# Performance work log

Hardware: AMD Instinct MI355X
Metric: run time of the kernel (lower is better)

The kernel has to match this reference:

```python
import jax, jax.numpy as jnp
from jax import lax
import numpy as np

# Mamba2 config from PixelMamba.__init__
D_MODEL = 128; D_STATE = 256; D_CONV = 4; EXPAND = 4; HEADDIM = 32
D_INNER = EXPAND * D_MODEL              # 512
NHEADS = D_INNER // HEADDIM             # 16
NGROUPS = 1
D_XBC = D_INNER + 2 * NGROUPS * D_STATE # 1024 (conv channels)
D_IN_PROJ = 2 * D_INNER + 2 * NGROUPS * D_STATE + NHEADS  # 1552
CHUNK = 128                             # SSD chunk length


def setup_inputs() -> dict:
    key = jax.random.key(0)
    ks = jax.random.split(key, 10)
    Bb, C, H, W = 2, 3, 64, 64
    f32 = jnp.float32
    rn = lambda k, shape, s: jax.random.normal(k, shape, f32) * s
    return {
        "x": jax.random.normal(ks[0], (Bb, C, H, W), f32),
        "fc0_w": rn(ks[1], (3, D_MODEL), 1.0 / np.sqrt(3.0)),
        "fc0_b": rn(ks[2], (D_MODEL,), 0.01),
        "in_proj_w": rn(ks[3], (D_MODEL, D_IN_PROJ), 1.0 / np.sqrt(D_MODEL)),
        "conv_w": rn(ks[4], (D_XBC, D_CONV), 1.0 / np.sqrt(D_CONV)),
        "conv_b": rn(ks[5], (D_XBC,), 0.01),
        "dt_bias": jnp.log(jnp.expm1(jax.random.uniform(ks[6], (NHEADS,), f32, 0.001, 0.1))),
        "A_log": jnp.log(jax.random.uniform(ks[7], (NHEADS,), f32, 1.0, 16.0)),
        "D": rn(ks[8], (NHEADS,), 1.0),
        "norm_w": jnp.ones((D_INNER,), f32),
        "out_proj_w": rn(ks[9], (D_INNER, D_MODEL), 1.0 / np.sqrt(D_INNER)),
    }


def _mamba2(u, in_proj_w, conv_w, conv_b, dt_bias, A_log, D, norm_w, out_proj_w):
    # u: (B, L, d_model)
    Bb, L, _ = u.shape
    zxbcdt = u @ in_proj_w                                     # (B,L,1552)
    z = zxbcdt[..., :D_INNER]                                  # gate
    xBC = zxbcdt[..., D_INNER:D_INNER + D_XBC]
    dt = jax.nn.softplus(zxbcdt[..., -NHEADS:] + dt_bias)     # (B,L,H)

    # causal depthwise conv1d + SiLU
    xc = lax.conv_general_dilated(
        xBC.transpose(0, 2, 1), conv_w[:, None, :], (1,), [(D_CONV - 1, 0)],
        dimension_numbers=('NCH', 'OIH', 'NCH'), feature_group_count=D_XBC)
    xBC = jax.nn.silu(xc + conv_b[None, :, None]).transpose(0, 2, 1)

    xs = xBC[..., :D_INNER].reshape(Bb, L, NHEADS, HEADDIM)    # (B,L,H,P)
    Bm = xBC[..., D_INNER:D_INNER + D_STATE]                   # (B,L,N), ngroups=1
    Cm = xBC[..., D_INNER + D_STATE:]                          # (B,L,N)
    A = -jnp.exp(A_log)                                        # (H,) negative

    # ---- SSD chunked selective scan ----
    NC = L // CHUNK
    a = (dt * A).reshape(Bb, NC, CHUNK, NHEADS)                # log-decay per step (<=0)
    dt_r = dt.reshape(Bb, NC, CHUNK, NHEADS)
    x_r = xs.reshape(Bb, NC, CHUNK, NHEADS, HEADDIM)
    B_r = Bm.reshape(Bb, NC, CHUNK, D_STATE)
    C_r = Cm.reshape(Bb, NC, CHUNK, D_STATE)
    cum = jnp.cumsum(a, axis=2)                                # (B,NC,Q,H)

    # intra-chunk quadratic part: attn[t,s] = (C_t.B_s) * exp(cum_t - cum_s) * dt_s, s<=t
    mask = jnp.tril(jnp.ones((CHUNK, CHUNK), bool))
    diff = cum[:, :, :, None, :] - cum[:, :, None, :, :]       # (B,NC,t,s,H)
    decay = jnp.exp(jnp.where(mask[None, None, :, :, None], diff, -jnp.inf))
    CB = jnp.einsum('bctn,bcsn->bcts', C_r, B_r)
    attn = CB[..., None] * decay * dt_r[:, :, None, :, :]      # (B,NC,t,s,H)
    y_intra = jnp.einsum('bctsh,bcshp->bcthp', attn, x_r)

    # per-chunk end states: sum_s exp(cum_end - cum_s) dt_s x_s B_s^T
    decay_end = jnp.exp(cum[:, :, -1:, :] - cum)               # (B,NC,Q,H)
    states = jnp.einsum('bcsh,bcsn,bcshp->bchpn', decay_end * dt_r, B_r, x_r)

    # inter-chunk recurrence over NC chunks (small sequential scan)
    chunk_decay = jnp.exp(cum[:, :, -1, :])                    # (B,NC,H)
    def step(S, inp):
        cd, st = inp
        return S * cd[..., None, None] + st, S                 # emit state BEFORE chunk
    S0 = jnp.zeros((Bb, NHEADS, HEADDIM, D_STATE), u.dtype)
    _, prev = lax.scan(step, S0, (chunk_decay.transpose(1, 0, 2),
                                  states.transpose(1, 0, 2, 3, 4)))
    prev = prev.transpose(1, 0, 2, 3, 4)                       # (B,NC,H,P,N)
    y_inter = jnp.einsum('bcth,bctn,bchpn->bcthp', jnp.exp(cum), C_r, prev)

    y = (y_intra + y_inter).reshape(Bb, L, NHEADS, HEADDIM) + D[None, None, :, None] * xs
    y = y.reshape(Bb, L, D_INNER)

    # gated RMSNorm (norm_before_gate=False): norm(y * silu(z)) * w
    y = y * jax.nn.silu(z)
    y = y * lax.rsqrt(jnp.mean(y * y, axis=-1, keepdims=True) + 1e-5) * norm_w
    return y @ out_proj_w


def reference(x, fc0_w, fc0_b, in_proj_w, conv_w, conv_b, dt_bias, A_log, D, norm_w, out_proj_w):
    Bb, C, H, W = x.shape
    x1 = x.transpose(0, 2, 3, 1).reshape(Bb, -1, C)            # raster order
    x2 = x[:, :, ::-1, ::-1].transpose(0, 2, 3, 1).reshape(Bb, -1, C)  # flipped
    u = jnp.concatenate([x1, x2], axis=1) @ fc0_w + fc0_b      # (B, 2HW, 128)
    return _mamba2(u, in_proj_w, conv_w, conv_b, dt_bias, A_log, D, norm_w, out_proj_w)
```

## Files before the change

### kernel.cpp

```cpp
#include <hip/hip_runtime.h>

typedef short short8 __attribute__((ext_vector_type(8)));
typedef float f32x4 __attribute__((ext_vector_type(4)));
typedef unsigned short ushort;
typedef unsigned int uint;

#define MFMA16(a,b,c) __builtin_amdgcn_mfma_f32_16x16x32_bf16(a,b,c,0,0,0)
#define DPROJ 1552

constexpr size_t OFF_M    = 0;
constexpr size_t OFF_CB_B = 0x5000;
constexpr size_t OFF_WT   = 0x8000;
constexpr size_t OFF_XT   = 0x30000;
constexpr size_t OFF_DT   = OFF_XT  + 16777216ull;
constexpr size_t OFF_BCM  = OFF_DT  + 1048576ull;
constexpr size_t OFF_CUM  = OFF_BCM + 16777216ull;
constexpr size_t OFF_CDC  = OFF_CUM + 1048576ull;
constexpr size_t OFF_CBT  = OFF_CDC + 8192ull;
constexpr size_t OFF_BT   = OFF_CBT + 4194304ull;
constexpr size_t OFF_ST   = OFF_BT  + 8388608ull;
constexpr size_t OFF_Y    = OFF_ST  + 33554432ull;

__device__ __forceinline__ float sigm(float x){ return 1.0f/(1.0f + __expf(-x)); }
__device__ __forceinline__ ushort f2bf(float f){
  union { float f; uint u; } c; c.f = f;
  uint u = c.u;
  return (ushort)((u + 0x7FFFu + ((u>>16)&1u)) >> 16);
}
__device__ __forceinline__ float bf2f(ushort h){
  union { uint u; float f; } c; c.u = ((uint)h)<<16;
  return c.f;
}
__device__ __forceinline__ void swz2048(int p, int& bc, int& h){
  int xcd = p & 7, slot = p >> 3;
  bc = xcd*16 + (slot >> 4);
  h  = slot & 15;
}

__global__ __launch_bounds__(256) void k0_prep(const float* __restrict__ fc0_w,
                                               const float* __restrict__ fc0_b,
                                               const float* __restrict__ W,
                                               char* __restrict__ wsb){
  float* Mo = (float*)(wsb + OFF_M);
  float* Co = (float*)(wsb + OFF_CB_B);
  int j = blockIdx.x*256 + threadIdx.x;
  if (j >= DPROJ) return;
  float m0=0.f,m1=0.f,m2=0.f,cc=0.f;
  for (int d=0; d<128; ++d){
    float w = W[(size_t)d*DPROJ + j];
    m0 = fmaf(fc0_w[d],     w, m0);
    m1 = fmaf(fc0_w[128+d], w, m1);
    m2 = fmaf(fc0_w[256+d], w, m2);
    cc = fmaf(fc0_b[d],     w, cc);
  }
  Mo[j] = m0; Mo[DPROJ + j] = m1; Mo[2*DPROJ + j] = m2;
  Co[j] = cc;
}

__global__ __launch_bounds__(256) void k0b_wt(const float* __restrict__ norm_w,
                                              const float* __restrict__ Wout,
                                              char* __restrict__ wsb){
  ushort* WT = (ushort*)(wsb + OFF_WT);
  int d = blockIdx.x;
  for (int i = threadIdx.x; i < 512; i += 256)
    WT[(size_t)d*512 + i] = f2bf(norm_w[i]*Wout[(size_t)i*128 + d]);
}

__device__ __forceinline__ void proj8(int li, const float* __restrict__ xb,
                                      const float* m0, const float* m1, const float* m2,
                                      const float* c8, float* dst){
  if (li < 0){
    #pragma unroll
    for (int j=0;j<8;++j) dst[j] = 0.f;
    return;
  }
  int hh, wv;
  if (li < 4096){ hh = li>>6; wv = li&63; }
  else { int l2 = li-4096; hh = 63-(l2>>6); wv = 63-(l2&63); }
  float x0 = xb[hh*64+wv], x1 = xb[4096+hh*64+wv], x2 = xb[8192+hh*64+wv];
  #pragma unroll
  for (int j=0;j<8;++j)
    dst[j] = fmaf(x2, m2[j], fmaf(x1, m1[j], fmaf(x0, m0[j], c8[j])));
}

__device__ __forceinline__ void conv8(const float* cb8, const float* cw0, const float* cw1,
                                      const float* cw2, const float* cw3,
                                      const float* wA, const float* wB,
                                      const float* wC, const float* wD, ushort* o){
  #pragma unroll
  for (int j=0;j<8;++j){
    float a = cb8[j];
    a = fmaf(wA[j], cw0[j], a);
    a = fmaf(wB[j], cw1[j], a);
    a = fmaf(wC[j], cw2[j], a);
    a = fmaf(wD[j], cw3[j], a);
    o[j] = f2bf(a * sigm(a));
  }
}
__device__ __forceinline__ void cp8(ushort* d, const ushort* s){
  #pragma unroll
  for (int j=0;j<8;++j) d[j] = s[j];
}

__global__ __launch_bounds__(256) void k12_projconv(const float* __restrict__ x,
                                                    const float* __restrict__ conv_w,
                                                    const float* __restrict__ conv_b,
                                                    char* __restrict__ wsb){
  int tid = threadIdx.x;
  int cg = tid & 127, rl = tid >> 7;
  int row0 = blockIdx.x*16 + rl*8;
  int b = row0 >> 13, l0 = row0 & 8191;
  const float* M  = (const float*)(wsb + OFF_M);
  const float* Cc = (const float*)(wsb + OFF_CB_B);
  const float* xb = x + (size_t)b*12288;
  int ch0 = cg*8, j0 = 512 + ch0;
  float m0[8],m1[8],m2[8],c8[8],cw0[8],cw1[8],cw2[8],cw3[8],cb8[8];
  #pragma unroll
  for (int j=0;j<8;++j){
    m0[j]=M[j0+j]; m1[j]=M[DPROJ+j0+j]; m2[j]=M[2*DPROJ+j0+j]; c8[j]=Cc[j0+j];
    cw0[j]=conv_w[(ch0+j)*4+0]; cw1[j]=conv_w[(ch0+j)*4+1];
    cw2[j]=conv_w[(ch0+j)*4+2]; cw3[j]=conv_w[(ch0+j)*4+3];
    cb8[j]=conv_b[ch0+j];
  }
  bool is_xs = (ch0 < 512);
  ushort* bcmp = (ushort*)(wsb + OFF_BCM);
  int chb = ch0 - 512;
  uint colw[8][4];
  ushort oprev[8];
  float w0[8],w1[8],w2[8],w3[8];
  ushort o[8];
  proj8(l0-3, xb, m0,m1,m2,c8, w1);
  proj8(l0-2, xb, m0,m1,m2,c8, w2);
  proj8(l0-1, xb, m0,m1,m2,c8, w3);

#define ROW_EVEN(R, WN, WA, WB, WC)                                          \
  proj8(l0+R, xb, m0,m1,m2,c8, WN);                                          \
  conv8(cb8,cw0,cw1,cw2,cw3, WA,WB,WC,WN, o);                                \
  if (is_xs) cp8(oprev, o);                                                  \
  else *(uint4*)(bcmp + (size_t)(row0+R)*512 + chb) = *(uint4*)o;
#define ROW_ODD(R, WN, WA, WB, WC)                                           \
  proj8(l0+R, xb, m0,m1,m2,c8, WN);                                          \
  conv8(cb8,cw0,cw1,cw2,cw3, WA,WB,WC,WN, o);                                \
  if (is_xs){ _Pragma("unroll")                                              \
    for (int j=0;j<8;++j) colw[j][(R)>>1] = (uint)oprev[j] | ((uint)o[j]<<16); } \
  else *(uint4*)(bcmp + (size_t)(row0+R)*512 + chb) = *(uint4*)o;

  ROW_EVEN(0, w0, w1,w2,w3)
  ROW_ODD (1, w1, w2,w3,w0)
  ROW_EVEN(2, w2, w3,w0,w1)
  ROW_ODD (3, w3, w0,w1,w2)
  ROW_EVEN(4, w0, w1,w2,w3)
  ROW_ODD (5, w1, w2,w3,w0)
  ROW_EVEN(6, w2, w3,w0,w1)
  ROW_ODD (7, w3, w0,w1,w2)
#undef ROW_EVEN
#undef ROW_ODD

  if (is_xs){
    int h = ch0>>5, p0 = ch0&31;
    int bc = row0>>7, grp = (row0&127)>>3;
    ushort* dst = (ushort*)(wsb+OFF_XT) + (((size_t)(bc*16+h)*16 + grp)*32)*8;
    #pragma unroll
    for (int j=0;j<8;++j){
      uint4 v; v.x = colw[j][0]; v.y = colw[j][1]; v.z = colw[j][2]; v.w = colw[j][3];
      *(uint4*)(dst + (size_t)(p0+j)*8) = v;
    }
  }
}

__global__ __launch_bounds__(128) void k3_cum(const float* __restrict__ x,
                                              const float* __restrict__ dt_bias,
                                              const float* __restrict__ A_log,
                                              char* __restrict__ wsb){
  int bi = blockIdx.x;
  int h = bi & 15; int bc = bi >> 4;
  int t = threadIdx.x;
  int r = bc*128 + t;
  int b = r >> 13, l = r & 8191;
  int hp, wv;
  if (l < 4096){ hp = l>>6; wv = l&63; }
  else { int l2 = l-4096; hp = 63-(l2>>6); wv = 63-(l2&63); }
  const float* xb = x + (size_t)b*12288;
  float x0 = xb[hp*64+wv], x1 = xb[4096+hp*64+wv], x2 = xb[8192+hp*64+wv];
  const float* M  = (const float*)(wsb + OFF_M);
  const float* Cc = (const float*)(wsb + OFF_CB_B);
  int j = 1536 + h;
  float v = Cc[j];
  v = fmaf(x0, M[j], v);
  v = fmaf(x1, M[DPROJ+j], v);
  v = fmaf(x2, M[2*DPROJ+j], v);
  float tt = v + dt_bias[h];
  float dtv = (tt > 20.f) ? tt : log1pf(__expf(tt));
  ((float*)(wsb+OFF_DT))[(size_t)r*16 + h] = dtv;
  __shared__ float s[128];
  float A = -__expf(A_log[h]);
  s[t] = dtv * A; __syncthreads();
  for (int off=1; off<128; off<<=1){
    float sv = (t>=off) ? s[t-off] : 0.f;
    __syncthreads();
    s[t] += sv;
    __syncthreads();
  }
  ((float*)(wsb + OFF_CUM))[(size_t)bi*128 + t] = s[t];
  if (t==127) ((float*)(wsb + OFF_CDC))[bi] = __expf(s[127]);
}

__global__ __launch_bounds__(256) void k4a_cb(char* __restrict__ wsb){
  int bi = blockIdx.x;
  int sq = bi & 3; int bc = bi >> 2;
  __shared__ __align__(16) char sC[16384];
  __shared__ __align__(16) char sB[4096];
  const ushort* bcm = (const ushort*)(wsb + OFF_BCM);
  ushort* cbtT = (ushort*)(wsb + OFF_CBT) + (size_t)bc*16384;
  ushort* btb  = (ushort*)(wsb + OFF_BT)  + (size_t)bc*32768;
  size_t rb = (size_t)bc*128;
  int tid = threadIdx.x;
  int lane = tid&63, wid = tid>>6, l15 = lane&15, l4 = lane>>4;
  int s_base = sq*32;
  f32x4 acc[2][2] = {};
  for (int nt = 0; nt < 4; ++nt){
    int n0 = nt*64;
    __syncthreads();
    for (int idx = tid; idx < 1024; idx += 256){
      int t = idx>>3, c = idx&7;
      uint4 v = *(const uint4*)(bcm + (rb+t)*512 + 256 + n0 + c*8);
      *(uint4*)(sC + ((t*128 + c*16) ^ ((t&7)<<4))) = v;
    }
    {
      int idx = tid;
      int s = idx>>3, c = idx&7;
      uint4 v = *(const uint4*)(bcm + (rb+s_base+s)*512 + n0 + c*8);
      *(uint4*)(sB + ((s*128 + c*16) ^ ((s&7)<<4))) = v;
    }
    __syncthreads();
    {
      int grp_l = tid>>6, n_l = tid&63;
      ushort o[8];
      #pragma unroll
      for (int sj=0; sj<8; ++sj){
        int sl = grp_l*8 + sj;
        o[sj] = *(const ushort*)(sB + ((sl*128 + n_l*2) ^ ((sl&7)<<4)));
      }
      *(uint4*)(btb + (size_t)((sq*4+grp_l)*256 + n0 + n_l)*8) = *(uint4*)o;
    }
    #pragma unroll
    for (int ks = 0; ks < 2; ++ks){
      int kb = ks*64 + l4*16;
      int t0 = wid*32 + l15, t1 = t0 + 16;
      short8 a0 = *(const short8*)(sC + ((t0*128 + kb) ^ ((t0&7)<<4)));
      short8 a1 = *(const short8*)(sC + ((t1*128 + kb) ^ ((t1&7)<<4)));
      short8 b0 = *(const short8*)(sB + ((l15*128 + kb) ^ ((l15&7)<<4)));
      short8 b1 = *(const short8*)(sB + (((16+l15)*128 + kb) ^ (((16+l15)&7)<<4)));
      acc[0][0] = MFMA16(a0,b0,acc[0][0]);
      acc[0][1] = MFMA16(a0,b1,acc[0][1]);
      acc[1][0] = MFMA16(a1,b0,acc[1][0]);
      acc[1][1] = MFMA16(a1,b1,acc[1][1]);
    }
  }
  #pragma unroll
  for (int mt=0; mt<2; ++mt)
  #pragma unroll
  for (int st=0; st<2; ++st)
  #pragma unroll
  for (int r=0; r<4; ++r){
    int t = wid*32 + mt*16 + l4*4 + r;
    int s = s_base + st*16 + l15;
    cbtT[(size_t)((s>>3)*128 + t)*8 + (s&7)] = f2bf(acc[mt][st][r]);
  }
}

__global__ __launch_bounds__(256) void k4s_states(char* __restrict__ wsb){
  int bc, h; swz2048(blockIdx.x, bc, h);
  int bi = bc*16 + h;
  __shared__ float sW[128];
  const ushort* xt  = (const ushort*)(wsb + OFF_XT) + (size_t)bi*4096;
  const ushort* btb = (const ushort*)(wsb + OFF_BT) + (size_t)bc*32768;
  const float* cum  = (const float*)(wsb + OFF_CUM) + (size_t)bi*128;
  const float* dtp  = (const float*)(wsb + OFF_DT);
  ushort* st = (ushort*)(wsb + OFF_ST) + (size_t)bi*8192;
  size_t rb = (size_t)bc*128;
  int tid = threadIdx.x;
  if (tid < 128){
    float c127 = cum[127];
    sW[tid] = __expf(c127 - cum[tid]) * dtp[(rb+tid)*16 + h];
  }
  __syncthreads();
  int lane = tid&63, wid = tid>>6, l15 = lane&15, l4 = lane>>4;
  f32x4 acc2[2][4] = {};
  #pragma unroll
  for (int ks = 0; ks < 4; ++ks){
    int grp = ks*4 + l4;
    const float* wp = sW + grp*8;
    short8 ra0 = *(const short8*)(xt + (size_t)(grp*32 + l15)*8);
    short8 ra1 = *(const short8*)(xt + (size_t)(grp*32 + 16 + l15)*8);
    short8 a0, a1;
    #pragma unroll
    for (int j=0;j<8;++j){
      a0[j] = (short)f2bf(bf2f((ushort)ra0[j]) * wp[j]);
      a1[j] = (short)f2bf(bf2f((ushort)ra1[j]) * wp[j]);
    }
    #pragma unroll
    for (int ntl = 0; ntl < 4; ++ntl){
      int n = wid*64 + ntl*16 + l15;
      short8 b = *(const short8*)(btb + (size_t)(grp*256 + n)*8);
      acc2[0][ntl] = MFMA16(a0,b,acc2[0][ntl]);
      acc2[1][ntl] = MFMA16(a1,b,acc2[1][ntl]);
    }
  }
  #pragma unroll
  for (int mt=0; mt<2; ++mt)
  #pragma unroll
  for (int ntl=0; ntl<4; ++ntl)
  #pragma unroll
  for (int r=0; r<4; ++r){
    int p = mt*16 + l4*4 + r;
    int n = wid*64 + ntl*16 + l15;
    st[(size_t)((n>>3)*32 + p)*8 + (n&7)] = f2bf(acc2[mt][ntl][r]);
  }
}

__global__ __launch_bounds__(256) void k5_scan(char* __restrict__ wsb){
  int g = blockIdx.x*256 + threadIdx.x;
  int l = g & 63;
  int e = l & 7, plow = l >> 3;
  int up = g >> 6;
  int p = (up & 3)*8 + plow; up >>= 2;
  int grp = up & 31; up >>= 5;
  int h = up & 15; int b = up >> 4;
  int off = (grp*32 + p)*8 + e;
  ushort* st = (ushort*)(wsb + OFF_ST);
  const float* cdc = (const float*)(wsb + OFF_CDC);
  float S = 0.f;
  for (int c=0; c<64; ++c){
    int bi = (b*64+c)*16 + h;
    size_t idx = (size_t)bi*8192 + off;
    float v = bf2f(st[idx]);
    st[idx] = f2bf(S);
    S = fmaf(S, cdc[bi], v);
  }
}

__global__ __launch_bounds__(256) void k4y_out(const float* __restrict__ Dp,
                                               char* __restrict__ wsb){
  int bc, h; swz2048(blockIdx.x, bc, h);
  int bi = bc*16 + h;
  __shared__ float sCum[128], sDt[128], sE[128];
  const ushort* cbt = (const ushort*)(wsb + OFF_CBT) + (size_t)bc*16384;
  const ushort* xt  = (const ushort*)(wsb + OFF_XT) + (size_t)bi*4096;
  const ushort* bcm = (const ushort*)(wsb + OFF_BCM);
  const ushort* prev= (const ushort*)(wsb + OFF_ST) + (size_t)bi*8192;
  const float* cum  = (const float*)(wsb + OFF_CUM) + (size_t)bi*128;
  const float* dtp  = (const float*)(wsb + OFF_DT);
  ushort* Yb = (ushort*)(wsb + OFF_Y);
  size_t rb = (size_t)bc*128;
  int tid = threadIdx.x;
  if (tid < 128){
    float cv = cum[tid];
    sCum[tid] = cv;
    sDt[tid]  = dtp[(rb+tid)*16 + h];
    sE[tid]   = __expf(cv);
  }
  __syncthreads();
  int lane = tid&63, wid = tid>>6, l15 = lane&15, l4 = lane>>4;
  int t0 = wid*32 + l15, t1 = t0 + 16;
  float ct0 = sCum[t0], ct1 = sCum[t1];
  f32x4 acc[2][2] = {};
  #pragma unroll
  for (int ks = 0; ks < 4; ++ks){
    int grp = ks*4 + l4;
    int s0 = grp*8;
    short8 ra0 = *(const short8*)(cbt + (size_t)(grp*128 + t0)*8);
    short8 ra1 = *(const short8*)(cbt + (size_t)(grp*128 + t1)*8);
    short8 a0, a1;
    #pragma unroll
    for (int j=0;j<8;++j){
      int s = s0 + j;
      float cs = sCum[s], ds = sDt[s];
      float e0 = __expf(fminf(ct0 - cs, 0.f)) * ds;
      float e1 = __expf(fminf(ct1 - cs, 0.f)) * ds;
      float v0 = (t0 >= s) ? bf2f((ushort)ra0[j]) * e0 : 0.f;
      float v1 = (t1 >= s) ? bf2f((ushort)ra1[j]) * e1 : 0.f;
      a0[j] = (short)f2bf(v0);
      a1[j] = (short)f2bf(v1);
    }
    short8 b0 = *(const short8*)(xt + (size_t)(grp*32 + l15)*8);
    short8 b1 = *(const short8*)(xt + (size_t)(grp*32 + 16 + l15)*8);
    acc[0][0] = MFMA16(a0,b0,acc[0][0]);
    acc[0][1] = MFMA16(a0,b1,acc[0][1]);
    acc[1][0] = MFMA16(a1,b0,acc[1][0]);
    acc[1][1] = MFMA16(a1,b1,acc[1][1]);
  }
  f32x4 acc2[2][2] = {};
  #pragma unroll
  for (int ks = 0; ks < 8; ++ks){
    int koff = ks*32 + l4*8;
    int grp = ks*4 + l4;
    short8 a0 = *(const short8*)(bcm + (rb+t0)*512 + 256 + koff);
    short8 a1 = *(const short8*)(bcm + (rb+t1)*512 + 256 + koff);
    short8 b0 = *(const short8*)(prev + (size_t)(grp*32 + l15)*8);
    short8 b1 = *(const short8*)(prev + (size_t)(grp*32 + 16 + l15)*8);
    acc2[0][0] = MFMA16(a0,b0,acc2[0][0]);
    acc2[0][1] = MFMA16(a0,b1,acc2[0][1]);
    acc2[1][0] = MFMA16(a1,b0,acc2[1][0]);
    acc2[1][1] = MFMA16(a1,b1,acc2[1][1]);
  }
  float Dh = Dp[h];
  #pragma unroll
  for (int mt=0; mt<2; ++mt){
    int tb = wid*32 + mt*16 + l4*4;
    int tg = tb>>3, e0 = tb&7;
    #pragma unroll
    for (int nt=0; nt<2; ++nt){
      int p = nt*16 + l15;
      ushort xv[4];
      *(uint2*)xv = *(const uint2*)(xt + (size_t)(tg*32 + p)*8 + e0);
      #pragma unroll
      for (int r=0; r<4; ++r){
        int t = tb + r;
        float yv = acc[mt][nt][r] + sE[t]*acc2[mt][nt][r] + Dh*bf2f(xv[r]);
        Yb[(rb+t)*512 + h*32 + p] = f2bf(yv);
      }
    }
  }
}

__global__ __launch_bounds__(256) void k7_final(const float* __restrict__ x,
                                                char* __restrict__ wsb,
                                                float* __restrict__ out){
  int r0 = blockIdx.x*32;
  __shared__ __align__(16) char sG[32768];
  __shared__ float sScale[32];
  const ushort* Yb = (const ushort*)(wsb + OFF_Y);
  const float* M  = (const float*)(wsb + OFF_M);
  const float* Cb = (const float*)(wsb + OFF_CB_B);
  const ushort* WT = (const ushort*)(wsb + OFF_WT);
  int tid = threadIdx.x;
  int r = tid>>3, li = tid&7;
  int row = r0 + r; int b = row>>13, l = row & 8191;
  int hh, wv;
  if (l < 4096){ hh = l>>6; wv = l&63; }
  else { int l2 = l-4096; hh = 63-(l2>>6); wv = 63-(l2&63); }
  const float* xb = x + (size_t)b*12288;
  float x0 = xb[hh*64+wv], x1 = xb[4096+hh*64+wv], x2 = xb[8192+hh*64+wv];
  float sq = 0.f;
  #pragma unroll
  for (int k = 0; k < 8; ++k){
    int i0 = li*64 + k*8;
    short8 yv = *(const short8*)(Yb + (size_t)row*512 + i0);
    ushort g8[8];
    #pragma unroll
    for (int j=0;j<8;++j){
      int i = i0 + j;
      float z = Cb[i];
      z = fmaf(x0, M[i], z);
      z = fmaf(x1, M[DPROJ+i], z);
      z = fmaf(x2, M[2*DPROJ+i], z);
      float g = bf2f((ushort)yv[j]) * z * sigm(z);
      sq = fmaf(g, g, sq);
      g8[j] = f2bf(g);
    }
    *(uint4*)(sG + ((r*1024 + i0*2) ^ ((r&7)<<4))) = *(uint4*)g8;
  }
  sq += __shfl_xor(sq, 1, 64);
  sq += __shfl_xor(sq, 2, 64);
  sq += __shfl_xor(sq, 4, 64);
  if (li == 0) sScale[r] = rsqrtf(sq*(1.f/512.f) + 1e-5f);
  __syncthreads();
  int lane = tid&63, wid = tid>>6, l15 = lane&15, l4 = lane>>4;
  f32x4 acc[2][2] = {};
  #pragma unroll
  for (int ks = 0; ks < 16; ++ks){
    int kb = ks*64 + l4*16;
    int rr0 = l15, rr1 = 16+l15;
    short8 a0 = *(const short8*)(sG + ((rr0*1024 + kb) ^ ((rr0&7)<<4)));
    short8 a1 = *(const short8*)(sG + ((rr1*1024 + kb) ^ ((rr1&7)<<4)));
    int koff = ks*32 + l4*8;
    short8 b0 = *(const short8*)(WT + (size_t)(wid*32 + l15)*512 + koff);
    short8 b1 = *(const short8*)(WT + (size_t)(wid*32 + 16 + l15)*512 + koff);
    acc[0][0] = MFMA16(a0,b0,acc[0][0]);
    acc[0][1] = MFMA16(a0,b1,acc[0][1]);
    acc[1][0] = MFMA16(a1,b0,acc[1][0]);
    acc[1][1] = MFMA16(a1,b1,acc[1][1]);
  }
  #pragma unroll
  for (int mt=0; mt<2; ++mt)
  #pragma unroll
  for (int nt=0; nt<2; ++nt)
  #pragma unroll
  for (int r4=0; r4<4; ++r4){
    int rr = mt*16 + l4*4 + r4;
    int d = wid*32 + nt*16 + l15;
    out[(size_t)(r0+rr)*128 + d] = acc[mt][nt][r4] * sScale[rr];
  }
}

extern "C" void kernel_launch(void* const* d_in, const int* in_sizes, int n_in,
                              void* d_out, int out_size, void* d_ws, size_t ws_size,
                              hipStream_t stream) {
  const float* x         = (const float*)d_in[0];
  const float* fc0_w     = (const float*)d_in[1];
  const float* fc0_b     = (const float*)d_in[2];
  const float* in_proj_w = (const float*)d_in[3];
  const float* conv_w    = (const float*)d_in[4];
  const float* conv_b    = (const float*)d_in[5];
  const float* dt_bias   = (const float*)d_in[6];
  const float* A_log     = (const float*)d_in[7];
  const float* Dp        = (const float*)d_in[8];
  const float* norm_w    = (const float*)d_in[9];
  const float* out_proj_w= (const float*)d_in[10];
  char* wsb  = (char*)d_ws;
  float* out = (float*)d_out;

  k0_prep<<<dim3(7),     dim3(256), 0, stream>>>(fc0_w, fc0_b, in_proj_w, wsb);
  k0b_wt <<<dim3(128),   dim3(256), 0, stream>>>(norm_w, out_proj_w, wsb);
  k12_projconv<<<dim3(1024), dim3(256), 0, stream>>>(x, conv_w, conv_b, wsb);
  k3_cum <<<dim3(2048),  dim3(128), 0, stream>>>(x, dt_bias, A_log, wsb);
  k4a_cb <<<dim3(512),   dim3(256), 0, stream>>>(wsb);
  k4s_states<<<dim3(2048), dim3(256), 0, stream>>>(wsb);
  k5_scan<<<dim3(1024),  dim3(256), 0, stream>>>(wsb);
  k4y_out<<<dim3(2048),  dim3(256), 0, stream>>>(Dp, wsb);
  k7_final<<<dim3(512),  dim3(256), 0, stream>>>(x, wsb, out);
}
```

Baseline: 152.8 us.

## Fuse chunk-state, inter-chunk scan and inter-chunk output into one sequential kernel

Replaces the separate chunk-state kernel, the global-memory scan kernel and the inter-chunk output matmul with one kernel, kscan. Each block (batch, head, half of headdim) walks all 64 chunks in order. It keeps the running state in fp32 shared memory and writes y_inter directly, so the 32MB bf16 state round trip and the separate prev-state pass go away. The B-transpose layout is now written in k12_projconv instead of k4a_cb. The cost is that the sequential loop runs on only 64 blocks, which leaves most CUs idle and exposes per-chunk load latency and barrier latency 64 times in a row.

```diff
diff --git a/kernel.cpp b/kernel.cpp
--- a/kernel.cpp
+++ b/kernel.cpp
@@ -97,10 +97,6 @@
     o[j] = f2bf(a * sigm(a));
   }
 }
-__device__ __forceinline__ void cp8(ushort* d, const ushort* s){
-  #pragma unroll
-  for (int j=0;j<8;++j) d[j] = s[j];
-}
 
 __global__ __launch_bounds__(256) void k12_projconv(const float* __restrict__ x,
                                                     const float* __restrict__ conv_w,
@@ -123,6 +119,8 @@
     cb8[j]=conv_b[ch0+j];
   }
   bool is_xs = (ch0 < 512);
+  bool is_b  = (ch0 >= 512) && (ch0 < 768);
+  bool pack  = is_xs || is_b;
   ushort* bcmp = (ushort*)(wsb + OFF_BCM);
   int chb = ch0 - 512;
   uint colw[8][4];
@@ -136,14 +134,15 @@
 #define ROW_EVEN(R, WN, WA, WB, WC)                                          \
   proj8(l0+R, xb, m0,m1,m2,c8, WN);                                          \
   conv8(cb8,cw0,cw1,cw2,cw3, WA,WB,WC,WN, o);                                \
-  if (is_xs) cp8(oprev, o);                                                  \
-  else *(uint4*)(bcmp + (size_t)(row0+R)*512 + chb) = *(uint4*)o;
+  if (pack){ _Pragma("unroll")                                               \
+    for (int j=0;j<8;++j) oprev[j] = o[j]; }                                 \
+  if (!is_xs) *(uint4*)(bcmp + (size_t)(row0+R)*512 + chb) = *(uint4*)o;
 #define ROW_ODD(R, WN, WA, WB, WC)                                           \
   proj8(l0+R, xb, m0,m1,m2,c8, WN);                                          \
   conv8(cb8,cw0,cw1,cw2,cw3, WA,WB,WC,WN, o);                                \
-  if (is_xs){ _Pragma("unroll")                                              \
+  if (pack){ _Pragma("unroll")                                               \
     for (int j=0;j<8;++j) colw[j][(R)>>1] = (uint)oprev[j] | ((uint)o[j]<<16); } \
-  else *(uint4*)(bcmp + (size_t)(row0+R)*512 + chb) = *(uint4*)o;
+  if (!is_xs) *(uint4*)(bcmp + (size_t)(row0+R)*512 + chb) = *(uint4*)o;
 
   ROW_EVEN(0, w0, w1,w2,w3)
   ROW_ODD (1, w1, w2,w3,w0)
@@ -156,14 +155,21 @@
 #undef ROW_EVEN
 #undef ROW_ODD
 
+  int bc = row0>>7, grp = (row0&127)>>3;
   if (is_xs){
     int h = ch0>>5, p0 = ch0&31;
-    int bc = row0>>7, grp = (row0&127)>>3;
     ushort* dst = (ushort*)(wsb+OFF_XT) + (((size_t)(bc*16+h)*16 + grp)*32)*8;
     #pragma unroll
     for (int j=0;j<8;++j){
       uint4 v; v.x = colw[j][0]; v.y = colw[j][1]; v.z = colw[j][2]; v.w = colw[j][3];
       *(uint4*)(dst + (size_t)(p0+j)*8) = v;
+    }
+  } else if (is_b){
+    ushort* btb = (ushort*)(wsb+OFF_BT) + (size_t)bc*32768;
+    #pragma unroll
+    for (int j=0;j<8;++j){
+      uint4 v; v.x = colw[j][0]; v.y = colw[j][1]; v.z = colw[j][2]; v.w = colw[j][3];
+      *(uint4*)(btb + (size_t)(grp*256 + chb + j)*8) = v;
     }
   }
 }
@@ -212,7 +218,6 @@
   __shared__ __align__(16) char sB[4096];
   const ushort* bcm = (const ushort*)(wsb + OFF_BCM);
   ushort* cbtT = (ushort*)(wsb + OFF_CBT) + (size_t)bc*16384;
-  ushort* btb  = (ushort*)(wsb + OFF_BT)  + (size_t)bc*32768;
   size_t rb = (size_t)bc*128;
   int tid = threadIdx.x;
   int lane = tid&63, wid = tid>>6, l15 = lane&15, l4 = lane>>4;
@@ -233,16 +238,6 @@
       *(uint4*)(sB + ((s*128 + c*16) ^ ((s&7)<<4))) = v;
     }
     __syncthreads();
-    {
-      int grp_l = tid>>6, n_l = tid&63;
-      ushort o[8];
-      #pragma unroll
-      for (int sj=0; sj<8; ++sj){
-        int sl = grp_l*8 + sj;
-        o[sj] = *(const ushort*)(sB + ((sl*128 + n_l*2) ^ ((sl&7)<<4)));
-      }
-      *(uint4*)(btb + (size_t)((sq*4+grp_l)*256 + n0 + n_l)*8) = *(uint4*)o;
-    }
     #pragma unroll
     for (int ks = 0; ks < 2; ++ks){
       int kb = ks*64 + l4*16;
@@ -269,74 +264,85 @@
   }
 }
 
-__global__ __launch_bounds__(256) void k4s_states(char* __restrict__ wsb){
-  int bc, h; swz2048(blockIdx.x, bc, h);
-  int bi = bc*16 + h;
-  __shared__ float sW[128];
-  const ushort* xt  = (const ushort*)(wsb + OFF_XT) + (size_t)bi*4096;
-  const ushort* btb = (const ushort*)(wsb + OFF_BT) + (size_t)bc*32768;
-  const float* cum  = (const float*)(wsb + OFF_CUM) + (size_t)bi*128;
+__global__ __launch_bounds__(512) void kscan(char* __restrict__ wsb){
+  int blk = blockIdx.x;
+  int ph = blk & 1, h = (blk>>1)&15, b = blk>>5;
+  __shared__ float sS[4096];
+  __shared__ __align__(16) char sSb[8192];
+  __shared__ float sW[128], sE[128];
+  const ushort* xtb = (const ushort*)(wsb + OFF_XT);
+  const ushort* btb0= (const ushort*)(wsb + OFF_BT);
+  const ushort* bcm = (const ushort*)(wsb + OFF_BCM);
+  const float* cumb = (const float*)(wsb + OFF_CUM);
   const float* dtp  = (const float*)(wsb + OFF_DT);
-  ushort* st = (ushort*)(wsb + OFF_ST) + (size_t)bi*8192;
-  size_t rb = (size_t)bc*128;
+  const float* cdcp = (const float*)(wsb + OFF_CDC);
+  ushort* YI = (ushort*)(wsb + OFF_ST);
   int tid = threadIdx.x;
-  if (tid < 128){
-    float c127 = cum[127];
-    sW[tid] = __expf(c127 - cum[tid]) * dtp[(rb+tid)*16 + h];
-  }
+  int lane = tid&63, wave = tid>>6, l15 = lane&15, l4 = lane>>4;
+  for (int i = tid; i < 4096; i += 512) sS[i] = 0.f;
+  for (int i = tid; i < 4096; i += 512) ((ushort*)sSb)[i] = 0;
   __syncthreads();
-  int lane = tid&63, wid = tid>>6, l15 = lane&15, l4 = lane>>4;
-  f32x4 acc2[2][4] = {};
-  #pragma unroll
-  for (int ks = 0; ks < 4; ++ks){
-    int grp = ks*4 + l4;
-    const float* wp = sW + grp*8;
-    short8 ra0 = *(const short8*)(xt + (size_t)(grp*32 + l15)*8);
-    short8 ra1 = *(const short8*)(xt + (size_t)(grp*32 + 16 + l15)*8);
-    short8 a0, a1;
-    #pragma unroll
-    for (int j=0;j<8;++j){
-      a0[j] = (short)f2bf(bf2f((ushort)ra0[j]) * wp[j]);
-      a1[j] = (short)f2bf(bf2f((ushort)ra1[j]) * wp[j]);
-    }
-    #pragma unroll
-    for (int ntl = 0; ntl < 4; ++ntl){
-      int n = wid*64 + ntl*16 + l15;
-      short8 b = *(const short8*)(btb + (size_t)(grp*256 + n)*8);
-      acc2[0][ntl] = MFMA16(a0,b,acc2[0][ntl]);
-      acc2[1][ntl] = MFMA16(a1,b,acc2[1][ntl]);
-    }
-  }
-  #pragma unroll
-  for (int mt=0; mt<2; ++mt)
-  #pragma unroll
-  for (int ntl=0; ntl<4; ++ntl)
-  #pragma unroll
-  for (int r=0; r<4; ++r){
-    int p = mt*16 + l4*4 + r;
-    int n = wid*64 + ntl*16 + l15;
-    st[(size_t)((n>>3)*32 + p)*8 + (n&7)] = f2bf(acc2[mt][ntl][r]);
-  }
-}
-
-__global__ __launch_bounds__(256) void k5_scan(char* __restrict__ wsb){
-  int g = blockIdx.x*256 + threadIdx.x;
-  int l = g & 63;
-  int e = l & 7, plow = l >> 3;
-  int up = g >> 6;
-  int p = (up & 3)*8 + plow; up >>= 2;
-  int grp = up & 31; up >>= 5;
-  int h = up & 15; int b = up >> 4;
-  int off = (grp*32 + p)*8 + e;
-  ushort* st = (ushort*)(wsb + OFF_ST);
-  const float* cdc = (const float*)(wsb + OFF_CDC);
-  float S = 0.f;
-  for (int c=0; c<64; ++c){
-    int bi = (b*64+c)*16 + h;
-    size_t idx = (size_t)bi*8192 + off;
-    float v = bf2f(st[idx]);
-    st[idx] = f2bf(S);
-    S = fmaf(S, cdc[bi], v);
+  for (int c = 0; c < 64; ++c){
+    int bcc = b*64 + c;
+    int bi = bcc*16 + h;
+    size_t rb = (size_t)bcc*128;
+    if (tid < 128){
+      float cv = cumb[(size_t)bi*128 + tid];
+      float c127 = cumb[(size_t)bi*128 + 127];
+      sW[tid] = __expf(c127 - cv) * dtp[(rb+tid)*16 + h];
+      sE[tid] = __expf(cv);
+    }
+    __syncthreads();
+    const ushort* xt  = xtb + (size_t)bi*4096;
+    const ushort* btb = btb0 + (size_t)bcc*32768;
+    f32x4 accY = {};
+    #pragma unroll
+    for (int ks = 0; ks < 8; ++ks){
+      short8 a = *(const short8*)(bcm + (rb + wave*16 + l15)*512 + 256 + ks*32 + l4*8);
+      short8 bS = *(const short8*)(sSb + ((l15*512 + ks*64 + l4*16) ^ ((l15&7)<<4)));
+      accY = MFMA16(a, bS, accY);
+    }
+    f32x4 accS[2] = {};
+    #pragma unroll
+    for (int ks = 0; ks < 4; ++ks){
+      int grp = ks*4 + l4;
+      const float* wp = sW + grp*8;
+      short8 rx = *(const short8*)(xt + (size_t)(grp*32 + ph*16 + l15)*8);
+      short8 ax;
+      #pragma unroll
+      for (int j=0;j<8;++j) ax[j] = (short)f2bf(bf2f((ushort)rx[j]) * wp[j]);
+      #pragma unroll
+      for (int nt2 = 0; nt2 < 2; ++nt2){
+        int n = wave*32 + nt2*16 + l15;
+        short8 bB = *(const short8*)(btb + (size_t)(grp*256 + n)*8);
+        accS[nt2] = MFMA16(ax, bB, accS[nt2]);
+      }
+    }
+    #pragma unroll
+    for (int r = 0; r < 4; ++r){
+      int t = wave*16 + l4*4 + r;
+      YI[(size_t)bi*4096 + t*32 + ph*16 + l15] = f2bf(accY[r] * sE[t]);
+    }
+    float cd = cdcp[bi];
+    #pragma unroll
+    for (int nt2 = 0; nt2 < 2; ++nt2)
+    #pragma unroll
+    for (int r = 0; r < 4; ++r){
+      int p = l4*4 + r;
+      int n = wave*32 + nt2*16 + l15;
+      int a = p*256 + n;
+      sS[a] = fmaf(sS[a], cd, accS[nt2][r]);
+    }
+    __syncthreads();
+    {
+      int i0 = tid*8;
+      int p = i0 >> 8, n = i0 & 255;
+      ushort o[8];
+      #pragma unroll
+      for (int j=0;j<8;++j) o[j] = f2bf(sS[i0+j]);
+      *(uint4*)(sSb + ((p*512 + n*2) ^ ((p&7)<<4))) = *(uint4*)o;
+    }
+    __syncthreads();
   }
 }
 
@@ -344,21 +350,18 @@
                                                char* __restrict__ wsb){
   int bc, h; swz2048(blockIdx.x, bc, h);
   int bi = bc*16 + h;
-  __shared__ float sCum[128], sDt[128], sE[128];
+  __shared__ float sCum[128], sDt[128];
   const ushort* cbt = (const ushort*)(wsb + OFF_CBT) + (size_t)bc*16384;
   const ushort* xt  = (const ushort*)(wsb + OFF_XT) + (size_t)bi*4096;
-  const ushort* bcm = (const ushort*)(wsb + OFF_BCM);
-  const ushort* prev= (const ushort*)(wsb + OFF_ST) + (size_t)bi*8192;
+  const ushort* YIp = (const ushort*)(wsb + OFF_ST) + (size_t)bi*4096;
   const float* cum  = (const float*)(wsb + OFF_CUM) + (size_t)bi*128;
   const float* dtp  = (const float*)(wsb + OFF_DT);
   ushort* Yb = (ushort*)(wsb + OFF_Y);
   size_t rb = (size_t)bc*128;
   int tid = threadIdx.x;
   if (tid < 128){
-    float cv = cum[tid];
-    sCum[tid] = cv;
+    sCum[tid] = cum[tid];
     sDt[tid]  = dtp[(rb+tid)*16 + h];
-    sE[tid]   = __expf(cv);
   }
   __syncthreads();
   int lane = tid&63, wid = tid>>6, l15 = lane&15, l4 = lane>>4;
@@ -390,20 +393,6 @@
     acc[1][0] = MFMA16(a1,b0,acc[1][0]);
     acc[1][1] = MFMA16(a1,b1,acc[1][1]);
   }
-  f32x4 acc2[2][2] = {};
-  #pragma unroll
-  for (int ks = 0; ks < 8; ++ks){
-    int koff = ks*32 + l4*8;
-    int grp = ks*4 + l4;
-    short8 a0 = *(const short8*)(bcm + (rb+t0)*512 + 256 + koff);
-    short8 a1 = *(const short8*)(bcm + (rb+t1)*512 + 256 + koff);
-    short8 b0 = *(const short8*)(prev + (size_t)(grp*32 + l15)*8);
-    short8 b1 = *(const short8*)(prev + (size_t)(grp*32 + 16 + l15)*8);
-    acc2[0][0] = MFMA16(a0,b0,acc2[0][0]);
-    acc2[0][1] = MFMA16(a0,b1,acc2[0][1]);
-    acc2[1][0] = MFMA16(a1,b0,acc2[1][0]);
-    acc2[1][1] = MFMA16(a1,b1,acc2[1][1]);
-  }
   float Dh = Dp[h];
   #pragma unroll
   for (int mt=0; mt<2; ++mt){
@@ -417,7 +406,8 @@
       #pragma unroll
       for (int r=0; r<4; ++r){
         int t = tb + r;
-        float yv = acc[mt][nt][r] + sE[t]*acc2[mt][nt][r] + Dh*bf2f(xv[r]);
+        float yi = bf2f(YIp[t*32 + p]);
+        float yv = acc[mt][nt][r] + yi + Dh*bf2f(xv[r]);
         Yb[(rb+t)*512 + h*32 + p] = f2bf(yv);
       }
     }
@@ -515,9 +505,8 @@
   k0b_wt <<<dim3(128),   dim3(256), 0, stream>>>(norm_w, out_proj_w, wsb);
   k12_projconv<<<dim3(1024), dim3(256), 0, stream>>>(x, conv_w, conv_b, wsb);
   k3_cum <<<dim3(2048),  dim3(128), 0, stream>>>(x, dt_bias, A_log, wsb);
+  kscan  <<<dim3(64),    dim3(512), 0, stream>>>(wsb);
   k4a_cb <<<dim3(512),   dim3(256), 0, stream>>>(wsb);
-  k4s_states<<<dim3(2048), dim3(256), 0, stream>>>(wsb);
-  k5_scan<<<dim3(1024),  dim3(256), 0, stream>>>(wsb);
   k4y_out<<<dim3(2048),  dim3(256), 0, stream>>>(Dp, wsb);
   k7_final<<<dim3(512),  dim3(256), 0, stream>>>(x, wsb, out);
 }
```

Result: slower. 372.6 us (+143.9%).
